# Performance work log

Measured on AMD Instinct MI355X. Metric: run time of the kernel, lower is better.

Reference implementation:

```python
import jax, jax.numpy as jnp
import numpy as np

B, N, DIN, DINNER, DOUT, W = 4, 8192, 512, 512, 512, 128


def setup_inputs() -> dict:
    key = jax.random.key(0)
    k1, k2, k3 = jax.random.split(key, 3)
    x = jax.random.normal(k1, (B, N, DIN), jnp.float32)
    # torch Linear weights: (out_features, in_features)
    w_qkv = jax.random.normal(k2, (3 * DINNER, DIN), jnp.float32) * (DIN ** -0.5)
    w_out = jax.random.normal(k3, (DOUT, DINNER), jnp.float32) * (DINNER ** -0.5)
    b_out = jnp.zeros((DOUT,), jnp.float32)
    return {"x": x, "w_qkv": w_qkv, "w_out": w_out, "b_out": b_out}


def reference(x, w_qkv, w_out, b_out):
    b, n, _ = x.shape
    w = W
    scale = DINNER ** -0.5
    pad = (-n) % w  # pad_to_multiple along seq dim (static)
    xp = jnp.pad(x, ((0, 0), (0, pad), (0, 0)))
    qkv = jnp.einsum('bnd,ed->bne', xp, w_qkv)  # to_qkv, no bias
    q, k, v = jnp.split(qkv, 3, axis=-1)
    win = lambda t: t.reshape(b, -1, w, DINNER)  # b (w n) d -> b w n d
    q, k, v = win(q), win(k), win(v)
    # prepend one zero bucket to k, then overlap prev/current windows.
    kp = jnp.pad(k, ((0, 0), (1, 0), (0, 0), (0, 0)))
    k2 = jnp.concatenate((kp[:, :-1], kp[:, 1:]), axis=2)  # (b, nb, 2w, d)
    # NOTE: source bug replicated — v is also built from k, not v.
    v2 = jnp.concatenate((kp[:, :-1], kp[:, 1:]), axis=2)
    sim = jnp.einsum('bwid,bwjd->bwij', q, k2) * scale  # (b, nb, w, 2w)
    i, j = w, 2 * w
    mask = jnp.triu(jnp.ones((i, j), bool), j - i + 1)
    sim = jnp.where(mask, -jnp.finfo(sim.dtype).max, sim)
    attn = jax.nn.softmax(sim, axis=-1)
    out = jnp.einsum('bwij,bwjd->bwid', attn, v2)
    out = out.reshape(b, -1, DINNER)[:, :n]
    return jnp.einsum('bnd,od->bno', out, w_out) + b_out
```

## Files before the change

### kernel.cpp

```cpp
#include <hip/hip_runtime.h>
#include <cstdint>
#include <cstddef>

typedef float f32x4 __attribute__((ext_vector_type(4)));
typedef short s16x8 __attribute__((ext_vector_type(8)));
typedef short s16x4 __attribute__((ext_vector_type(4)));

#define MFMA_BF16(a, b, c) __builtin_amdgcn_mfma_f32_16x16x32_bf16((a), (b), (c), 0, 0, 0)

__device__ __forceinline__ unsigned short f2bf(float f) {
  unsigned int u = __float_as_uint(f);
  u += 0x7FFFu + ((u >> 16) & 1u);
  return (unsigned short)(u >> 16);
}

__device__ __forceinline__ s16x8 cvt8(const float* __restrict__ src) {
  const float4 f0 = *(const float4*)src;
  const float4 f1 = *(const float4*)(src + 4);
  s16x8 h;
  h[0] = (short)f2bf(f0.x); h[1] = (short)f2bf(f0.y);
  h[2] = (short)f2bf(f0.z); h[3] = (short)f2bf(f0.w);
  h[4] = (short)f2bf(f1.x); h[5] = (short)f2bf(f1.y);
  h[6] = (short)f2bf(f1.z); h[7] = (short)f2bf(f1.w);
  return h;
}

__global__ __launch_bounds__(512, 2)
void gemm_qk(const float* __restrict__ x, const float* __restrict__ wqkv,
             unsigned short* __restrict__ Q, unsigned short* __restrict__ K) {
  __shared__ unsigned short As[128 * 72];
  __shared__ unsigned short Bs[256 * 72];
  const int t = threadIdx.x;
  const int m0 = blockIdx.y * 128;
  const int n0 = blockIdx.x * 256;
  const int wid = t >> 6, lane = t & 63;
  const int wm = wid >> 2, wn = wid & 3;
  const int nl = lane & 15, quad = lane >> 4;
  const int srow = t >> 3, scol = (t & 7) * 8;

  const f32x4 zero = {0.f, 0.f, 0.f, 0.f};
  f32x4 acc[4][4];
#pragma unroll
  for (int i = 0; i < 4; ++i)
#pragma unroll
    for (int j = 0; j < 4; ++j) acc[i][j] = zero;

  for (int kc = 0; kc < 512; kc += 64) {
#pragma unroll
    for (int p = 0; p < 2; ++p) {
      const int r = srow + p * 64;
      *(s16x8*)&As[r * 72 + scol] = cvt8(x + (size_t)(m0 + r) * 512 + kc + scol);
    }
#pragma unroll
    for (int p = 0; p < 4; ++p) {
      const int r = srow + p * 64;
      *(s16x8*)&Bs[r * 72 + scol] = cvt8(wqkv + (size_t)(n0 + r) * 512 + kc + scol);
    }
    __syncthreads();
#pragma unroll
    for (int ks = 0; ks < 2; ++ks) {
      s16x8 af[4], bf[4];
#pragma unroll
      for (int i = 0; i < 4; ++i)
        af[i] = *(const s16x8*)&As[(wm * 64 + i * 16 + nl) * 72 + ks * 32 + quad * 8];
#pragma unroll
      for (int j = 0; j < 4; ++j)
        bf[j] = *(const s16x8*)&Bs[(wn * 64 + j * 16 + nl) * 72 + ks * 32 + quad * 8];
#pragma unroll
      for (int i = 0; i < 4; ++i)
#pragma unroll
        for (int j = 0; j < 4; ++j) acc[i][j] = MFMA_BF16(af[i], bf[j], acc[i][j]);
    }
    __syncthreads();
  }
#pragma unroll
  for (int i = 0; i < 4; ++i) {
    const int mrow = m0 + wm * 64 + i * 16 + quad * 4;
#pragma unroll
    for (int j = 0; j < 4; ++j) {
      const int n = n0 + wn * 64 + j * 16 + nl;
      unsigned short* dst = (n < 512 ? Q : K) + (size_t)mrow * 512 + (n & 511);
#pragma unroll
      for (int r = 0; r < 4; ++r) dst[(size_t)r * 512] = f2bf(acc[i][j][r]);
    }
  }
}

__global__ __launch_bounds__(512, 2)
void gemm_kwt(const unsigned short* __restrict__ K, const float* __restrict__ wout,
              unsigned short* __restrict__ KWT) {
  __shared__ unsigned short As[128 * 72];
  __shared__ unsigned short Bs[256 * 72];
  const int t = threadIdx.x;
  const int m0 = blockIdx.y * 128;
  const int n0 = blockIdx.x * 256;
  const int wid = t >> 6, lane = t & 63;
  const int wm = wid >> 2, wn = wid & 3;
  const int nl = lane & 15, quad = lane >> 4;
  const int srow = t >> 3, scol = (t & 7) * 8;

  const f32x4 zero = {0.f, 0.f, 0.f, 0.f};
  f32x4 acc[4][4];
#pragma unroll
  for (int i = 0; i < 4; ++i)
#pragma unroll
    for (int j = 0; j < 4; ++j) acc[i][j] = zero;

  for (int kc = 0; kc < 512; kc += 64) {
#pragma unroll
    for (int p = 0; p < 2; ++p) {
      const int r = srow + p * 64;
      *(s16x8*)&As[r * 72 + scol] =
          *(const s16x8*)(K + (size_t)(m0 + r) * 512 + kc + scol);
    }
#pragma unroll
    for (int p = 0; p < 4; ++p) {
      const int r = srow + p * 64;
      *(s16x8*)&Bs[r * 72 + scol] = cvt8(wout + (size_t)(n0 + r) * 512 + kc + scol);
    }
    __syncthreads();
#pragma unroll
    for (int ks = 0; ks < 2; ++ks) {
      s16x8 af[4], bf[4];
#pragma unroll
      for (int i = 0; i < 4; ++i)
        af[i] = *(const s16x8*)&As[(wm * 64 + i * 16 + nl) * 72 + ks * 32 + quad * 8];
#pragma unroll
      for (int j = 0; j < 4; ++j)
        bf[j] = *(const s16x8*)&Bs[(wn * 64 + j * 16 + nl) * 72 + ks * 32 + quad * 8];
#pragma unroll
      for (int i = 0; i < 4; ++i)
#pragma unroll
        for (int j = 0; j < 4; ++j) acc[i][j] = MFMA_BF16(af[i], bf[j], acc[i][j]);
    }
    __syncthreads();
  }
#pragma unroll
  for (int i = 0; i < 4; ++i) {
    const int m = m0 + wm * 64 + i * 16 + quad * 4;
    const int b = m >> 13, ns = m & 8191;
#pragma unroll
    for (int j = 0; j < 4; ++j) {
      const int o = n0 + wn * 64 + j * 16 + nl;
      s16x4 h;
#pragma unroll
      for (int r = 0; r < 4; ++r) h[r] = (short)f2bf(acc[i][j][r]);
      *(s16x4*)&KWT[(size_t)(b * 512 + o) * 8192 + ns] = h;
    }
  }
}

__global__ __launch_bounds__(512, 2)
void attn_p(const unsigned short* __restrict__ Q, const unsigned short* __restrict__ K,
            unsigned short* __restrict__ P) {
  __shared__ unsigned short Qs[128 * 72];
  __shared__ unsigned short Ks[256 * 72];
  __shared__ float redm[128 * 4];
  __shared__ float reds[128 * 4];
  const int t = threadIdx.x;
  const int bx = blockIdx.x, b = bx >> 6, w = bx & 63;
  const int wid = t >> 6, lane = t & 63;
  const int wm = wid >> 2, wn = wid & 3;
  const int nl = lane & 15, quad = lane >> 4;
  const int srow = t >> 3, scol = (t & 7) * 8;

  const f32x4 zero = {0.f, 0.f, 0.f, 0.f};
  f32x4 acc[4][4];
#pragma unroll
  for (int i = 0; i < 4; ++i)
#pragma unroll
    for (int j = 0; j < 4; ++j) acc[i][j] = zero;

  const unsigned short* Qb = Q + (size_t)(b * 8192 + w * 128) * 512;
  const unsigned short* Kb = K + (size_t)(b * 8192) * 512;

  for (int kc = 0; kc < 512; kc += 64) {
#pragma unroll
    for (int p = 0; p < 2; ++p) {
      const int r = srow + p * 64;
      *(s16x8*)&Qs[r * 72 + scol] = *(const s16x8*)(Qb + (size_t)r * 512 + kc + scol);
    }
#pragma unroll
    for (int p = 0; p < 4; ++p) {
      const int r = srow + p * 64;
      int sq = w * 128 - 128 + r;
      if (sq < 0) sq = 0;
      *(s16x8*)&Ks[r * 72 + scol] = *(const s16x8*)(Kb + (size_t)sq * 512 + kc + scol);
    }
    __syncthreads();
#pragma unroll
    for (int ks = 0; ks < 2; ++ks) {
      s16x8 af[4], bf[4];
#pragma unroll
      for (int i = 0; i < 4; ++i)
        af[i] = *(const s16x8*)&Qs[(wm * 64 + i * 16 + nl) * 72 + ks * 32 + quad * 8];
#pragma unroll
      for (int j = 0; j < 4; ++j)
        bf[j] = *(const s16x8*)&Ks[(wn * 64 + j * 16 + nl) * 72 + ks * 32 + quad * 8];
#pragma unroll
      for (int i = 0; i < 4; ++i)
#pragma unroll
        for (int j = 0; j < 4; ++j) acc[i][j] = MFMA_BF16(af[i], bf[j], acc[i][j]);
    }
    __syncthreads();
  }

  const float scale = 0.04419417382415922f;
  float rmax[4][4];
#pragma unroll
  for (int i = 0; i < 4; ++i) {
#pragma unroll
    for (int r = 0; r < 4; ++r) {
      const int row = wm * 64 + i * 16 + quad * 4 + r;
      float mx = -3.4e38f;
#pragma unroll
      for (int j = 0; j < 4; ++j) {
        const int col = wn * 64 + j * 16 + nl;
        float v = acc[i][j][r] * scale;
        if (col >= 128 && col - 128 > row) v = -3.0e38f;
        if (w == 0 && col < 128) v = 0.0f;
        acc[i][j][r] = v;
        mx = fmaxf(mx, v);
      }
      rmax[i][r] = mx;
    }
  }
#pragma unroll
  for (int off = 1; off < 16; off <<= 1)
#pragma unroll
    for (int i = 0; i < 4; ++i)
#pragma unroll
      for (int r = 0; r < 4; ++r)
        rmax[i][r] = fmaxf(rmax[i][r], __shfl_xor(rmax[i][r], off, 64));
  if (nl == 0) {
#pragma unroll
    for (int i = 0; i < 4; ++i)
#pragma unroll
      for (int r = 0; r < 4; ++r)
        redm[(wm * 64 + i * 16 + quad * 4 + r) * 4 + wn] = rmax[i][r];
  }
  __syncthreads();
  float rsum[4][4];
#pragma unroll
  for (int i = 0; i < 4; ++i) {
#pragma unroll
    for (int r = 0; r < 4; ++r) {
      const f32x4 mv = *(const f32x4*)&redm[(wm * 64 + i * 16 + quad * 4 + r) * 4];
      const float m = fmaxf(fmaxf(mv[0], mv[1]), fmaxf(mv[2], mv[3]));
      rmax[i][r] = m;
      float s = 0.f;
#pragma unroll
      for (int j = 0; j < 4; ++j) {
        const float p = __expf(acc[i][j][r] - m);
        acc[i][j][r] = p;
        s += p;
      }
      rsum[i][r] = s;
    }
  }
#pragma unroll
  for (int off = 1; off < 16; off <<= 1)
#pragma unroll
    for (int i = 0; i < 4; ++i)
#pragma unroll
      for (int r = 0; r < 4; ++r) rsum[i][r] += __shfl_xor(rsum[i][r], off, 64);
  if (nl == 0) {
#pragma unroll
    for (int i = 0; i < 4; ++i)
#pragma unroll
      for (int r = 0; r < 4; ++r)
        reds[(wm * 64 + i * 16 + quad * 4 + r) * 4 + wn] = rsum[i][r];
  }
  __syncthreads();
#pragma unroll
  for (int i = 0; i < 4; ++i) {
#pragma unroll
    for (int r = 0; r < 4; ++r) {
      const int row = wm * 64 + i * 16 + quad * 4 + r;
      const f32x4 sv = *(const f32x4*)&reds[row * 4];
      const float inv = 1.0f / (sv[0] + sv[1] + sv[2] + sv[3]);
#pragma unroll
      for (int j = 0; j < 4; ++j) {
        const int col = wn * 64 + j * 16 + nl;
        float pv = acc[i][j][r] * inv;
        if (w == 0 && col < 128) pv = 0.0f;
        P[(size_t)bx * 32768 + (size_t)row * 256 + col] = f2bf(pv);
      }
    }
  }
}

__global__ __launch_bounds__(512, 2)
void gemm_out(const unsigned short* __restrict__ P, const unsigned short* __restrict__ KWT,
              const float* __restrict__ bias, float* __restrict__ out) {
  __shared__ unsigned short As[128 * 72];
  __shared__ unsigned short Bs[256 * 72];
  const int t = threadIdx.x;
  const int wbx = blockIdx.y, b = wbx >> 6, w = wbx & 63;
  const int o0 = blockIdx.x * 256;
  const int wid = t >> 6, lane = t & 63;
  const int wm = wid >> 2, wn = wid & 3;
  const int nl = lane & 15, quad = lane >> 4;
  const int srow = t >> 3, scol = (t & 7) * 8;

  const f32x4 zero = {0.f, 0.f, 0.f, 0.f};
  f32x4 acc[4][4];
#pragma unroll
  for (int i = 0; i < 4; ++i)
#pragma unroll
    for (int j = 0; j < 4; ++j) acc[i][j] = zero;

  const unsigned short* Pw = P + (size_t)wbx * 32768;
  const int seqbase = w * 128 - 128;

  for (int kc = 0; kc < 256; kc += 64) {
#pragma unroll
    for (int p = 0; p < 2; ++p) {
      const int r = srow + p * 64;
      *(s16x8*)&As[r * 72 + scol] = *(const s16x8*)(Pw + (size_t)r * 256 + kc + scol);
    }
#pragma unroll
    for (int p = 0; p < 4; ++p) {
      const int r = srow + p * 64;
      const int o = o0 + r;
      int sq = seqbase + kc + scol;
      if (sq < 0) sq = 0;
      *(s16x8*)&Bs[r * 72 + scol] =
          *(const s16x8*)(KWT + (size_t)(b * 512 + o) * 8192 + sq);
    }
    __syncthreads();
#pragma unroll
    for (int ks = 0; ks < 2; ++ks) {
      s16x8 af[4], bf[4];
#pragma unroll
      for (int i = 0; i < 4; ++i)
        af[i] = *(const s16x8*)&As[(wm * 64 + i * 16 + nl) * 72 + ks * 32 + quad * 8];
#pragma unroll
      for (int j = 0; j < 4; ++j)
        bf[j] = *(const s16x8*)&Bs[(wn * 64 + j * 16 + nl) * 72 + ks * 32 + quad * 8];
#pragma unroll
      for (int i = 0; i < 4; ++i)
#pragma unroll
        for (int j = 0; j < 4; ++j) acc[i][j] = MFMA_BF16(af[i], bf[j], acc[i][j]);
    }
    __syncthreads();
  }
#pragma unroll
  for (int i = 0; i < 4; ++i) {
    const int row = wm * 64 + i * 16 + quad * 4;
#pragma unroll
    for (int j = 0; j < 4; ++j) {
      const int o = o0 + wn * 64 + j * 16 + nl;
      const float bo = bias[o];
      float* dst = out + (size_t)(b * 8192 + w * 128 + row) * 512 + o;
#pragma unroll
      for (int r = 0; r < 4; ++r) dst[(size_t)r * 512] = acc[i][j][r] + bo;
    }
  }
}

extern "C" void kernel_launch(void* const* d_in, const int* in_sizes, int n_in,
                              void* d_out, int out_size, void* d_ws, size_t ws_size,
                              hipStream_t stream) {
  const float* x = (const float*)d_in[0];
  const float* w_qkv = (const float*)d_in[1];
  const float* w_out = (const float*)d_in[2];
  const float* b_out = (const float*)d_in[3];
  float* out = (float*)d_out;

  char* ws = (char*)d_ws;
  unsigned short* Q = (unsigned short*)ws;
  unsigned short* K = (unsigned short*)(ws + (size_t)33554432);
  unsigned short* KWT = (unsigned short*)(ws + (size_t)67108864);
  unsigned short* P = (unsigned short*)(ws + (size_t)100663296);

  const dim3 blk(512);
  gemm_qk<<<dim3(4, 256), blk, 0, stream>>>(x, w_qkv, Q, K);
  gemm_kwt<<<dim3(2, 256), blk, 0, stream>>>(K, w_out, KWT);
  attn_p<<<dim3(256), blk, 0, stream>>>(Q, K, P);
  gemm_out<<<dim3(2, 256), blk, 0, stream>>>(P, KWT, b_out, out);
}
```

Baseline: 286.8 us.

## Pre-convert inputs to bf16 and stage GEMM tiles via direct global-to-LDS loads

Adds a separate pass that converts x, w_qkv and w_out to bf16 once, instead of converting fp32 to bf16 inside every GEMM tile load. All four kernels now fill shared memory with global_load_lds 16-byte direct loads into an unpadded, XOR-swizzled layout that avoids LDS bank conflicts. The two projection GEMMs shrink to 128x128 tiles with 256 threads, and the occupancy hint of 2 is dropped from the launch bounds. The cost is an extra kernel launch and a full pass over x, plus workspace aliasing (xb shares space with KWT, and the weights share space with P) that depends on kernel order. One rmax assignment in the softmax is also removed.

```diff
diff --git a/kernel.cpp b/kernel.cpp
--- a/kernel.cpp
+++ b/kernel.cpp
@@ -7,6 +7,11 @@
 typedef short s16x4 __attribute__((ext_vector_type(4)));
 
 #define MFMA_BF16(a, b, c) __builtin_amdgcn_mfma_f32_16x16x32_bf16((a), (b), (c), 0, 0, 0)
+
+#define GLD16(g, l)                                                            \
+  __builtin_amdgcn_global_load_lds(                                            \
+      (const __attribute__((address_space(1))) void*)(g),                      \
+      (__attribute__((address_space(3))) void*)(l), 16, 0, 0)
 
 __device__ __forceinline__ unsigned short f2bf(float f) {
   unsigned int u = __float_as_uint(f);
@@ -25,18 +30,34 @@
   return h;
 }
 
-__global__ __launch_bounds__(512, 2)
-void gemm_qk(const float* __restrict__ x, const float* __restrict__ wqkv,
+#define XN 16777216
+#define WQN 524288
+#define WON 262144
+__global__ __launch_bounds__(256)
+void cvt_bf16(const float* __restrict__ x, const float* __restrict__ wqkv,
+              const float* __restrict__ wout, unsigned short* __restrict__ xb,
+              unsigned short* __restrict__ wb, unsigned short* __restrict__ wob) {
+  const size_t i = (size_t)(blockIdx.x * 256 + threadIdx.x) * 8;
+  const float* src;
+  unsigned short* dst;
+  if (i < XN) { src = x + i; dst = xb + i; }
+  else if (i < XN + WQN) { src = wqkv + (i - XN); dst = wb + (i - XN); }
+  else { src = wout + (i - XN - WQN); dst = wob + (i - XN - WQN); }
+  *(s16x8*)dst = cvt8(src);
+}
+
+__global__ __launch_bounds__(256)
+void gemm_qk(const unsigned short* __restrict__ xb, const unsigned short* __restrict__ wb,
              unsigned short* __restrict__ Q, unsigned short* __restrict__ K) {
-  __shared__ unsigned short As[128 * 72];
-  __shared__ unsigned short Bs[256 * 72];
+  __shared__ unsigned short As[128 * 64];
+  __shared__ unsigned short Bs[128 * 64];
   const int t = threadIdx.x;
-  const int m0 = blockIdx.y * 128;
-  const int n0 = blockIdx.x * 256;
-  const int wid = t >> 6, lane = t & 63;
-  const int wm = wid >> 2, wn = wid & 3;
+  const int lane = t & 63, wid = t >> 6;
+  const int wm = wid >> 1, wn = wid & 1;
   const int nl = lane & 15, quad = lane >> 4;
-  const int srow = t >> 3, scol = (t & 7) * 8;
+  const int m0 = blockIdx.y * 128, n0 = blockIdx.x * 128;
+  const int sub = lane >> 3;
+  const int lblk = (lane & 7) ^ sub;
 
   const f32x4 zero = {0.f, 0.f, 0.f, 0.f};
   f32x4 acc[4][4];
@@ -45,16 +66,14 @@
 #pragma unroll
     for (int j = 0; j < 4; ++j) acc[i][j] = zero;
 
+  const unsigned short* gA = xb + (size_t)(m0 + wid * 32 + sub) * 512 + lblk * 8;
+  const unsigned short* gB = wb + (size_t)(n0 + wid * 32 + sub) * 512 + lblk * 8;
+
   for (int kc = 0; kc < 512; kc += 64) {
 #pragma unroll
-    for (int p = 0; p < 2; ++p) {
-      const int r = srow + p * 64;
-      *(s16x8*)&As[r * 72 + scol] = cvt8(x + (size_t)(m0 + r) * 512 + kc + scol);
-    }
-#pragma unroll
-    for (int p = 0; p < 4; ++p) {
-      const int r = srow + p * 64;
-      *(s16x8*)&Bs[r * 72 + scol] = cvt8(wqkv + (size_t)(n0 + r) * 512 + kc + scol);
+    for (int ii = 0; ii < 4; ++ii) {
+      GLD16(gA + kc + (size_t)(ii * 8) * 512, &As[(wid * 32 + ii * 8) * 64]);
+      GLD16(gB + kc + (size_t)(ii * 8) * 512, &Bs[(wid * 32 + ii * 8) * 64]);
     }
     __syncthreads();
 #pragma unroll
@@ -62,10 +81,12 @@
       s16x8 af[4], bf[4];
 #pragma unroll
       for (int i = 0; i < 4; ++i)
-        af[i] = *(const s16x8*)&As[(wm * 64 + i * 16 + nl) * 72 + ks * 32 + quad * 8];
+        af[i] = *(const s16x8*)&As[(wm * 64 + i * 16 + nl) * 64 +
+                                   (((ks * 4 + quad) ^ (nl & 7)) * 8)];
 #pragma unroll
       for (int j = 0; j < 4; ++j)
-        bf[j] = *(const s16x8*)&Bs[(wn * 64 + j * 16 + nl) * 72 + ks * 32 + quad * 8];
+        bf[j] = *(const s16x8*)&Bs[(wn * 64 + j * 16 + nl) * 64 +
+                                   (((ks * 4 + quad) ^ (nl & 7)) * 8)];
 #pragma unroll
       for (int i = 0; i < 4; ++i)
 #pragma unroll
@@ -86,18 +107,17 @@
   }
 }
 
-__global__ __launch_bounds__(512, 2)
-void gemm_kwt(const unsigned short* __restrict__ K, const float* __restrict__ wout,
+__global__ __launch_bounds__(256)
+void gemm_kwt(const unsigned short* __restrict__ K, const unsigned short* __restrict__ wob,
               unsigned short* __restrict__ KWT) {
-  __shared__ unsigned short As[128 * 72];
-  __shared__ unsigned short Bs[256 * 72];
+  __shared__ unsigned short As[128 * 64];
+  __shared__ unsigned short Bs[128 * 64];
   const int t = threadIdx.x;
-  const int m0 = blockIdx.y * 128;
-  const int n0 = blockIdx.x * 256;
-  const int wid = t >> 6, lane = t & 63;
-  const int wm = wid >> 2, wn = wid & 3;
+  const int lane = t & 63, wid = t >> 6;
+  const int wm = wid >> 1, wn = wid & 1;
   const int nl = lane & 15, quad = lane >> 4;
-  const int srow = t >> 3, scol = (t & 7) * 8;
+  const int m0 = blockIdx.y * 128, n0 = blockIdx.x * 128;
+  const int sub = lane >> 3, lblk = (lane & 7) ^ sub;
 
   const f32x4 zero = {0.f, 0.f, 0.f, 0.f};
   f32x4 acc[4][4];
@@ -106,17 +126,14 @@
 #pragma unroll
     for (int j = 0; j < 4; ++j) acc[i][j] = zero;
 
+  const unsigned short* gA = K + (size_t)(m0 + wid * 32 + sub) * 512 + lblk * 8;
+  const unsigned short* gB = wob + (size_t)(n0 + wid * 32 + sub) * 512 + lblk * 8;
+
   for (int kc = 0; kc < 512; kc += 64) {
 #pragma unroll
-    for (int p = 0; p < 2; ++p) {
-      const int r = srow + p * 64;
-      *(s16x8*)&As[r * 72 + scol] =
-          *(const s16x8*)(K + (size_t)(m0 + r) * 512 + kc + scol);
-    }
-#pragma unroll
-    for (int p = 0; p < 4; ++p) {
-      const int r = srow + p * 64;
-      *(s16x8*)&Bs[r * 72 + scol] = cvt8(wout + (size_t)(n0 + r) * 512 + kc + scol);
+    for (int ii = 0; ii < 4; ++ii) {
+      GLD16(gA + kc + (size_t)(ii * 8) * 512, &As[(wid * 32 + ii * 8) * 64]);
+      GLD16(gB + kc + (size_t)(ii * 8) * 512, &Bs[(wid * 32 + ii * 8) * 64]);
     }
     __syncthreads();
 #pragma unroll
@@ -124,10 +141,12 @@
       s16x8 af[4], bf[4];
 #pragma unroll
       for (int i = 0; i < 4; ++i)
-        af[i] = *(const s16x8*)&As[(wm * 64 + i * 16 + nl) * 72 + ks * 32 + quad * 8];
+        af[i] = *(const s16x8*)&As[(wm * 64 + i * 16 + nl) * 64 +
+                                   (((ks * 4 + quad) ^ (nl & 7)) * 8)];
 #pragma unroll
       for (int j = 0; j < 4; ++j)
-        bf[j] = *(const s16x8*)&Bs[(wn * 64 + j * 16 + nl) * 72 + ks * 32 + quad * 8];
+        bf[j] = *(const s16x8*)&Bs[(wn * 64 + j * 16 + nl) * 64 +
+                                   (((ks * 4 + quad) ^ (nl & 7)) * 8)];
 #pragma unroll
       for (int i = 0; i < 4; ++i)
 #pragma unroll
@@ -150,19 +169,19 @@
   }
 }
 
-__global__ __launch_bounds__(512, 2)
+__global__ __launch_bounds__(512)
 void attn_p(const unsigned short* __restrict__ Q, const unsigned short* __restrict__ K,
             unsigned short* __restrict__ P) {
-  __shared__ unsigned short Qs[128 * 72];
-  __shared__ unsigned short Ks[256 * 72];
+  __shared__ unsigned short Qs[128 * 64];
+  __shared__ unsigned short Ks[256 * 64];
   __shared__ float redm[128 * 4];
   __shared__ float reds[128 * 4];
   const int t = threadIdx.x;
   const int bx = blockIdx.x, b = bx >> 6, w = bx & 63;
-  const int wid = t >> 6, lane = t & 63;
+  const int lane = t & 63, wid = t >> 6;
   const int wm = wid >> 2, wn = wid & 3;
   const int nl = lane & 15, quad = lane >> 4;
-  const int srow = t >> 3, scol = (t & 7) * 8;
+  const int sub = lane >> 3, lblk = (lane & 7) ^ sub;
 
   const f32x4 zero = {0.f, 0.f, 0.f, 0.f};
   f32x4 acc[4][4];
@@ -176,16 +195,14 @@
 
   for (int kc = 0; kc < 512; kc += 64) {
 #pragma unroll
-    for (int p = 0; p < 2; ++p) {
-      const int r = srow + p * 64;
-      *(s16x8*)&Qs[r * 72 + scol] = *(const s16x8*)(Qb + (size_t)r * 512 + kc + scol);
-    }
-#pragma unroll
-    for (int p = 0; p < 4; ++p) {
-      const int r = srow + p * 64;
-      int sq = w * 128 - 128 + r;
+    for (int ii = 0; ii < 2; ++ii)
+      GLD16(Qb + (size_t)(wid * 16 + ii * 8 + sub) * 512 + kc + lblk * 8,
+            &Qs[(wid * 16 + ii * 8) * 64]);
+#pragma unroll
+    for (int ii = 0; ii < 4; ++ii) {
+      int sq = w * 128 - 128 + wid * 32 + ii * 8 + sub;
       if (sq < 0) sq = 0;
-      *(s16x8*)&Ks[r * 72 + scol] = *(const s16x8*)(Kb + (size_t)sq * 512 + kc + scol);
+      GLD16(Kb + (size_t)sq * 512 + kc + lblk * 8, &Ks[(wid * 32 + ii * 8) * 64]);
     }
     __syncthreads();
 #pragma unroll
@@ -193,10 +210,12 @@
       s16x8 af[4], bf[4];
 #pragma unroll
       for (int i = 0; i < 4; ++i)
-        af[i] = *(const s16x8*)&Qs[(wm * 64 + i * 16 + nl) * 72 + ks * 32 + quad * 8];
+        af[i] = *(const s16x8*)&Qs[(wm * 64 + i * 16 + nl) * 64 +
+                                   (((ks * 4 + quad) ^ (nl & 7)) * 8)];
 #pragma unroll
       for (int j = 0; j < 4; ++j)
-        bf[j] = *(const s16x8*)&Ks[(wn * 64 + j * 16 + nl) * 72 + ks * 32 + quad * 8];
+        bf[j] = *(const s16x8*)&Ks[(wn * 64 + j * 16 + nl) * 64 +
+                                   (((ks * 4 + quad) ^ (nl & 7)) * 8)];
 #pragma unroll
       for (int i = 0; i < 4; ++i)
 #pragma unroll
@@ -247,7 +266,6 @@
     for (int r = 0; r < 4; ++r) {
       const f32x4 mv = *(const f32x4*)&redm[(wm * 64 + i * 16 + quad * 4 + r) * 4];
       const float m = fmaxf(fmaxf(mv[0], mv[1]), fmaxf(mv[2], mv[3]));
-      rmax[i][r] = m;
       float s = 0.f;
 #pragma unroll
       for (int j = 0; j < 4; ++j) {
@@ -290,18 +308,18 @@
   }
 }
 
-__global__ __launch_bounds__(512, 2)
+__global__ __launch_bounds__(512)
 void gemm_out(const unsigned short* __restrict__ P, const unsigned short* __restrict__ KWT,
               const float* __restrict__ bias, float* __restrict__ out) {
-  __shared__ unsigned short As[128 * 72];
-  __shared__ unsigned short Bs[256 * 72];
+  __shared__ unsigned short As[128 * 64];
+  __shared__ unsigned short Bs[256 * 64];
   const int t = threadIdx.x;
   const int wbx = blockIdx.y, b = wbx >> 6, w = wbx & 63;
   const int o0 = blockIdx.x * 256;
-  const int wid = t >> 6, lane = t & 63;
+  const int lane = t & 63, wid = t >> 6;
   const int wm = wid >> 2, wn = wid & 3;
   const int nl = lane & 15, quad = lane >> 4;
-  const int srow = t >> 3, scol = (t & 7) * 8;
+  const int sub = lane >> 3, lblk = (lane & 7) ^ sub;
 
   const f32x4 zero = {0.f, 0.f, 0.f, 0.f};
   f32x4 acc[4][4];
@@ -315,29 +333,27 @@
 
   for (int kc = 0; kc < 256; kc += 64) {
 #pragma unroll
-    for (int p = 0; p < 2; ++p) {
-      const int r = srow + p * 64;
-      *(s16x8*)&As[r * 72 + scol] = *(const s16x8*)(Pw + (size_t)r * 256 + kc + scol);
-    }
-#pragma unroll
-    for (int p = 0; p < 4; ++p) {
-      const int r = srow + p * 64;
-      const int o = o0 + r;
-      int sq = seqbase + kc + scol;
-      if (sq < 0) sq = 0;
-      *(s16x8*)&Bs[r * 72 + scol] =
-          *(const s16x8*)(KWT + (size_t)(b * 512 + o) * 8192 + sq);
-    }
+    for (int ii = 0; ii < 2; ++ii)
+      GLD16(Pw + (size_t)(wid * 16 + ii * 8 + sub) * 256 + kc + lblk * 8,
+            &As[(wid * 16 + ii * 8) * 64]);
+    int sq = seqbase + kc + lblk * 8;
+    if (sq < 0) sq = 0;
+#pragma unroll
+    for (int ii = 0; ii < 4; ++ii)
+      GLD16(KWT + (size_t)(b * 512 + o0 + wid * 32 + ii * 8 + sub) * 8192 + sq,
+            &Bs[(wid * 32 + ii * 8) * 64]);
     __syncthreads();
 #pragma unroll
     for (int ks = 0; ks < 2; ++ks) {
       s16x8 af[4], bf[4];
 #pragma unroll
       for (int i = 0; i < 4; ++i)
-        af[i] = *(const s16x8*)&As[(wm * 64 + i * 16 + nl) * 72 + ks * 32 + quad * 8];
+        af[i] = *(const s16x8*)&As[(wm * 64 + i * 16 + nl) * 64 +
+                                   (((ks * 4 + quad) ^ (nl & 7)) * 8)];
 #pragma unroll
       for (int j = 0; j < 4; ++j)
-        bf[j] = *(const s16x8*)&Bs[(wn * 64 + j * 16 + nl) * 72 + ks * 32 + quad * 8];
+        bf[j] = *(const s16x8*)&Bs[(wn * 64 + j * 16 + nl) * 64 +
+                                   (((ks * 4 + quad) ^ (nl & 7)) * 8)];
 #pragma unroll
       for (int i = 0; i < 4; ++i)
 #pragma unroll
@@ -371,12 +387,15 @@
   char* ws = (char*)d_ws;
   unsigned short* Q = (unsigned short*)ws;
   unsigned short* K = (unsigned short*)(ws + (size_t)33554432);
+  unsigned short* xb = (unsigned short*)(ws + (size_t)67108864);
   unsigned short* KWT = (unsigned short*)(ws + (size_t)67108864);
   unsigned short* P = (unsigned short*)(ws + (size_t)100663296);
-
-  const dim3 blk(512);
-  gemm_qk<<<dim3(4, 256), blk, 0, stream>>>(x, w_qkv, Q, K);
-  gemm_kwt<<<dim3(2, 256), blk, 0, stream>>>(K, w_out, KWT);
-  attn_p<<<dim3(256), blk, 0, stream>>>(Q, K, P);
-  gemm_out<<<dim3(2, 256), blk, 0, stream>>>(P, KWT, b_out, out);
-}
+  unsigned short* wb = (unsigned short*)(ws + (size_t)100663296);
+  unsigned short* wob = (unsigned short*)(ws + (size_t)100663296 + 1048576);
+
+  cvt_bf16<<<dim3(8576), dim3(256), 0, stream>>>(x, w_qkv, w_out, xb, wb, wob);
+  gemm_qk<<<dim3(8, 256), dim3(256), 0, stream>>>(xb, wb, Q, K);
+  gemm_kwt<<<dim3(4, 256), dim3(256), 0, stream>>>(K, wob, KWT);
+  attn_p<<<dim3(256), dim3(512), 0, stream>>>(Q, K, P);
+  gemm_out<<<dim3(2, 256), dim3(512), 0, stream>>>(P, KWT, b_out, out);
+}
```

Result: faster. 262.4 us (-8.5%).
